# Optimization experiments

Hardware: AMD Instinct MI355X
Metric: run time of the kernel (lower is better)

Reference implementation:

```python
import jax, jax.numpy as jnp
import numpy as np
from jax import lax

DN = ('NHWC', 'HWIO', 'NHWC')

def _conv(a, w):
    return lax.conv_general_dilated(a, w, (1, 1), 'SAME', dimension_numbers=DN)

def _hard_sigmoid(z):
    return jnp.clip(0.2 * z + 0.5, 0.0, 1.0)


def setup_inputs() -> dict:
    key = jax.random.key(0)
    ks = jax.random.split(key, 4)
    B, T, H, W, C, F, K = 2, 16, 64, 64, 64, 64, 3
    x = jax.random.normal(ks[0], (B, T, H, W, C), dtype=jnp.float32)
    Wx = jax.random.normal(ks[1], (K, K, C, 4 * F), dtype=jnp.float32) * (2.0 / (K * K * C)) ** 0.5
    Wh = jax.random.normal(ks[2], (K, K, F, 4 * F), dtype=jnp.float32) * (2.0 / (K * K * F)) ** 0.5
    b = jax.random.normal(ks[3], (4 * F,), dtype=jnp.float32) * 0.01
    gamma = jnp.ones((F,), dtype=jnp.float32)
    beta = jnp.zeros((F,), dtype=jnp.float32)
    moving_mean = jnp.zeros((F,), dtype=jnp.float32)
    moving_var = jnp.ones((F,), dtype=jnp.float32)
    return {"x": x, "Wx": Wx, "Wh": Wh, "b": b, "gamma": gamma,
            "beta": beta, "moving_mean": moving_mean, "moving_var": moving_var}


def reference(x, Wx, Wh, b, gamma, beta, moving_mean, moving_var):
    B, T, H, W, C = x.shape
    F = Wh.shape[2]
    # Precompute the input-to-gate convolutions for all timesteps in one big conv.
    xg = _conv(x.reshape(B * T, H, W, C), Wx) + b          # (B*T, H, W, 4F)
    xg = xg.reshape(B, T, H, W, 4 * F).transpose(1, 0, 2, 3, 4)  # (T, B, H, W, 4F)

    h0 = jnp.zeros((B, H, W, F), dtype=x.dtype)
    c0 = jnp.zeros((B, H, W, F), dtype=x.dtype)

    def step(carry, xt):
        h, c = carry
        z = xt + _conv(h, Wh)                               # (B, H, W, 4F)
        zi, zf, zg, zo = jnp.split(z, 4, axis=-1)           # Keras gate order: i, f, c, o
        i = _hard_sigmoid(zi)
        f = _hard_sigmoid(zf)
        g = jnp.tanh(zg)
        o = _hard_sigmoid(zo)
        c_new = f * c + i * g
        h_new = o * jnp.tanh(c_new)
        return (h_new, c_new), h_new

    _, hs = lax.scan(step, (h0, c0), xg)                    # (T, B, H, W, F)
    out = hs.transpose(1, 0, 2, 3, 4)                       # (B, T, H, W, F)

    # BatchNormalization in inference mode (training=False), eps=1e-3 (Keras default)
    eps = 1e-3
    inv = gamma * lax.rsqrt(moving_var + eps)
    out = out * inv + (beta - moving_mean * inv)
    return out
```

## Files before the change

### kernel.cpp

```cpp
#include <hip/hip_runtime.h>
#include <cstddef>

typedef __attribute__((ext_vector_type(8))) _Float16 half8;
typedef __attribute__((ext_vector_type(4))) float f32x4;
typedef __attribute__((ext_vector_type(4))) unsigned short us4;

#define TT 16
#define APAD 72
#define A_TILE (3*34*APAD)
#define CHUNK  8192
#define NB     6
#define PF     5
#define XNB    4
#define XPF    3

__device__ __forceinline__ unsigned short f2h(float f) {
    return __builtin_bit_cast(unsigned short, (_Float16)f);
}
__device__ __forceinline__ float h2f(unsigned short u) {
    return (float)__builtin_bit_cast(_Float16, u);
}
__device__ __forceinline__ float hsig(float z) {
    return fminf(fmaxf(0.2f * z + 0.5f, 0.f), 1.f);
}

__global__ __launch_bounds__(256) void prep_kernel(
    const float* __restrict__ Wx, const float* __restrict__ Wh,
    const float* __restrict__ gamma, const float* __restrict__ beta,
    const float* __restrict__ mean, const float* __restrict__ var,
    unsigned short* __restrict__ Wc, float* __restrict__ bn)
{
    if (blockIdx.x == 1152) {
        if (threadIdx.x < 64) {
            const int c = threadIdx.x;
            const float inv = gamma[c] * rsqrtf(var[c] + 1e-3f);
            bn[c] = inv;
            bn[64 + c] = beta[c] - mean[c] * inv;
        }
        return;
    }
    const int i = blockIdx.x * 256 + threadIdx.x;
    const int j  = i & 7;
    const int n  = (i >> 3) & 255;
    const int kg = (i >> 11) & 3;
    const int s  = i >> 13;
    const int sub = s % 18;
    const float* W = (s >= 18) ? Wh : Wx;
    const int k5 = sub * 32 + kg * 8 + j;
    const int c = k5 & 63, q = k5 >> 6;
    const int kx = q % 3, ky = q / 3;
    Wc[i] = f2h(W[(size_t)((ky * 3 + kx) * 64 + c) * 256 + n]);
}

#define BLOAD(slot, ci) {                                                     \
    const unsigned short* _p = Wc + (size_t)(ci) * CHUNK + boff;              \
    bp[slot][0] = *(const half8*)_p;                                          \
    bp[slot][1] = *(const half8*)(_p + 128);                                  \
}

template<int C0, int CLAST, int AOFF>
__device__ __forceinline__ void conv_pass18(
    const unsigned short* __restrict__ Wc, const int boff,
    half8 (&bp)[NB][2],
    const unsigned short* abase,
    f32x4 acc[2][2])
{
    #pragma unroll
    for (int sub = 0; sub < 18; ++sub) {
        const int ci = C0 + sub;
        if (ci + PF <= CLAST) BLOAD((ci + PF) % NB, ci + PF)

        const int ky = sub / 6, kx = (sub / 2) % 3, cb = sub & 1;
        const half8 b0 = bp[ci % NB][0];
        const half8 b1 = bp[ci % NB][1];
        const unsigned short* at = abase + AOFF + (ky * 34 + kx) * APAD + cb * 32;
        const half8 a0 = *(const half8*)(at);
        const half8 a1 = *(const half8*)(at + 16 * APAD);
        acc[0][0] = __builtin_amdgcn_mfma_f32_16x16x32_f16(a0, b0, acc[0][0], 0, 0, 0);
        acc[0][1] = __builtin_amdgcn_mfma_f32_16x16x32_f16(a0, b1, acc[0][1], 0, 0, 0);
        acc[1][0] = __builtin_amdgcn_mfma_f32_16x16x32_f16(a1, b0, acc[1][0], 0, 0, 0);
        acc[1][1] = __builtin_amdgcn_mfma_f32_16x16x32_f16(a1, b1, acc[1][1], 0, 0, 0);
    }
}

__global__ __launch_bounds__(512) void xconv_kernel(
    const float* __restrict__ x,
    const unsigned short* __restrict__ Wc,
    const float* __restrict__ bias,
    unsigned short* __restrict__ xg)
{
    const int bid0 = blockIdx.x;
    const int bid = (bid0 & 7) * 256 + (bid0 >> 3);
    const int y = bid & 63;
    const int t = (bid >> 6) & 15;
    const int n = bid >> 10;
    const int tid = threadIdx.x, lane = tid & 63, w = tid >> 6;
    const int p0 = lane & 15, g = lane >> 4;

    __shared__ __align__(16) unsigned short smem[3 * 66 * APAD];

    const int boff = g * 2048 + (w * 32 + p0) * 8;

    half8 bp[XNB][2];
    #pragma unroll
    for (int sc = 0; sc < XPF; ++sc) BLOAD(sc, sc)

    const float* __restrict__ xt = x + (size_t)(n * TT + t) * 4096 * 64;
    for (int idx = tid; idx < 3 * 66 * 8; idx += 512) {
        const int cg  = idx & 7;
        const int col = (idx >> 3) % 66;
        const int r   = (idx >> 3) / 66;
        const int gy = y + r - 1;
        const int gx = col - 1;
        const bool ok = ((unsigned)gy < 64u) && ((unsigned)gx < 64u);
        float4 v0 = make_float4(0.f, 0.f, 0.f, 0.f), v1 = v0;
        if (ok) {
            const float* p = xt + (size_t)(gy * 64 + gx) * 64 + cg * 8;
            v0 = *(const float4*)p;
            v1 = *(const float4*)(p + 4);
        }
        __align__(16) unsigned short os[8];
        os[0] = f2h(v0.x); os[1] = f2h(v0.y); os[2] = f2h(v0.z); os[3] = f2h(v0.w);
        os[4] = f2h(v1.x); os[5] = f2h(v1.y); os[6] = f2h(v1.z); os[7] = f2h(v1.w);
        *(uint4*)&smem[(r * 66 + col) * APAD + cg * 8] = *(const uint4*)os;
    }
    __syncthreads();

    const unsigned short* abase = smem + p0 * APAD + g * 8;

    f32x4 acc[4][2] = {};
    #pragma unroll
    for (int sub = 0; sub < 18; ++sub) {
        if (sub + XPF < 18) BLOAD((sub + XPF) % XNB, sub + XPF)

        const int ky = sub / 6, kx = (sub / 2) % 3, cb = sub & 1;
        const half8 b0 = bp[sub % XNB][0];
        const half8 b1 = bp[sub % XNB][1];
        #pragma unroll
        for (int cq = 0; cq < 4; ++cq) {
            const half8 a = *(const half8*)(abase
                + (ky * 66 + cq * 16 + kx) * APAD + cb * 32);
            acc[cq][0] = __builtin_amdgcn_mfma_f32_16x16x32_f16(a, b0, acc[cq][0], 0, 0, 0);
            acc[cq][1] = __builtin_amdgcn_mfma_f32_16x16x32_f16(a, b1, acc[cq][1], 0, 0, 0);
        }
    }

    const float bv0 = bias[w * 32 + p0];
    const float bv1 = bias[w * 32 + 16 + p0];
    #pragma unroll
    for (int xh2 = 0; xh2 < 2; ++xh2) {
        unsigned short os[16];
        #pragma unroll
        for (int mfc = 0; mfc < 2; ++mfc)
            #pragma unroll
            for (int nf = 0; nf < 2; ++nf)
                #pragma unroll
                for (int j = 0; j < 4; ++j)
                    os[mfc * 8 + nf * 4 + j] =
                        f2h(acc[xh2 * 2 + mfc][nf][j] + (nf ? bv1 : bv0));
        const size_t vi = ((((size_t)(n * TT + t) * 64 + y) * 2 + xh2) * 8 + w) * 64 + lane;
        unsigned short* dst = xg + vi * 16;
        *(uint4*)dst       = *(uint4*)&os[0];
        *(uint4*)(dst + 8) = *(uint4*)&os[8];
    }
}

template<int FUSED>
__global__ __launch_bounds__(512) void convstep_kernel(
    const float* __restrict__ x,
    const unsigned short* __restrict__ hb,
    const unsigned short* __restrict__ Wc,
    const float* __restrict__ bias,
    const unsigned short* __restrict__ xg,
    float* __restrict__ cbuf,
    unsigned short* __restrict__ ho,
    const float* __restrict__ bn,
    float* __restrict__ out,
    const int t)
{
    const int bid0 = blockIdx.x;
    const int bid = (bid0 & 7) * 32 + (bid0 >> 3);
    const int xh = bid & 1;
    const int y  = (bid >> 1) & 63;
    const int n  = bid >> 7;
    const int tid = threadIdx.x;
    const int lane = tid & 63;
    const int w = tid >> 6;
    const int p0 = lane & 15;
    const int g  = lane >> 4;

    constexpr int SMEM_SHORTS = FUSED ? (2 * A_TILE) : 17408;
    __shared__ __align__(16) unsigned short smem[SMEM_SHORTS];

    const int boff = g * 2048 + (w * 32 + p0) * 8;
    const bool do_h = FUSED || (t > 0);

    unsigned short xs[16];
    if (!FUSED) {
        const size_t vi = ((((size_t)(n * TT + t) * 64 + y) * 2 + xh) * 8 + w) * 64 + lane;
        const uint4* xp = (const uint4*)(xg + vi * 16);
        *(uint4*)&xs[0] = xp[0];
        *(uint4*)&xs[8] = xp[1];
    }

    f32x4 acc[2][2] = {};
    if (do_h) {
        constexpr int C0 = FUSED ? 0 : 18;
        half8 bp[NB][2];
        #pragma unroll
        for (int sc = 0; sc < PF; ++sc) BLOAD((C0 + sc) % NB, C0 + sc)

        constexpr int NTILE = FUSED ? 2 : 1;
        const float* __restrict__ xt = x + (size_t)(n * TT + t) * 4096 * 64;
        const size_t hbase = (size_t)n * 4096 * 64;
        for (int idx = tid; idx < NTILE * 3 * 34 * 8; idx += 512) {
            const int cg  = idx & 7;
            const int col = (idx >> 3) % 34;
            const int i3  = (idx >> 3) / 34;
            const int r   = i3 % 3;
            const int src = i3 / 3;
            const int gy = y + r - 1;
            const int gx = xh * 32 + col - 1;
            const bool ok = ((unsigned)gy < 64u) && ((unsigned)gx < 64u);
            const int ebase = (r * 34 + col) * APAD + cg * 8;
            if (FUSED && src == 0) {
                float4 v0 = make_float4(0.f, 0.f, 0.f, 0.f), v1 = v0;
                if (ok) {
                    const float* p = xt + (size_t)(gy * 64 + gx) * 64 + cg * 8;
                    v0 = *(const float4*)p;
                    v1 = *(const float4*)(p + 4);
                }
                __align__(16) unsigned short os[8];
                os[0] = f2h(v0.x); os[1] = f2h(v0.y); os[2] = f2h(v0.z); os[3] = f2h(v0.w);
                os[4] = f2h(v1.x); os[5] = f2h(v1.y); os[6] = f2h(v1.z); os[7] = f2h(v1.w);
                *(uint4*)&smem[ebase] = *(const uint4*)os;
            } else {
                uint4 v = make_uint4(0u, 0u, 0u, 0u);
                if (ok) v = *(const uint4*)(hb + hbase + (size_t)(gy * 64 + gx) * 64 + cg * 8);
                *(uint4*)&smem[(FUSED ? A_TILE : 0) + ebase] = v;
            }
        }
        __syncthreads();

        const unsigned short* abase = smem + p0 * APAD + g * 8;
        if (FUSED) {
            conv_pass18<0, 35, 0>(Wc, boff, bp, abase, acc);
            conv_pass18<18, 35, A_TILE>(Wc, boff, bp, abase, acc);
        } else {
            conv_pass18<18, 35, 0>(Wc, boff, bp, abase, acc);
        }
    }

    __syncthreads();
    float* gbuf = (float*)smem;
    const int gate = w >> 1;
    const int chalf = (w & 1) * 32;

    float bv[2];
    bv[0] = bias[w * 32 + p0];
    bv[1] = bias[w * 32 + 16 + p0];

    #pragma unroll
    for (int mf = 0; mf < 2; ++mf)
        #pragma unroll
        for (int nf = 0; nf < 2; ++nf)
            #pragma unroll
            for (int j = 0; j < 4; ++j) {
                float v = acc[mf][nf][j] + (FUSED ? bv[nf] : h2f(xs[mf * 8 + nf * 4 + j]));
                v = (gate == 2) ? tanhf(v) : hsig(v);
                const int px = mf * 16 + g * 4 + j;
                gbuf[(gate * 32 + px) * 68 + chalf + nf * 16 + p0] = v;
            }
    __syncthreads();

    const int p  = tid >> 4;
    const int c4 = (tid & 15) * 4;
    const float4 iv = *(const float4*)&gbuf[(0 * 32 + p) * 68 + c4];
    const float4 fv = *(const float4*)&gbuf[(1 * 32 + p) * 68 + c4];
    const float4 gv = *(const float4*)&gbuf[(2 * 32 + p) * 68 + c4];
    const float4 ov = *(const float4*)&gbuf[(3 * 32 + p) * 68 + c4];
    const size_t gpix = (size_t)((n * 64 + y) * 64 + xh * 32 + p);
    const size_t sb = gpix * 64 + c4;
    const float4 cold = do_h ? *(const float4*)&cbuf[sb]
                             : make_float4(0.f, 0.f, 0.f, 0.f);
    const float4 scv  = *(const float4*)&bn[c4];
    const float4 shv  = *(const float4*)&bn[64 + c4];

    const float ivv[4] = {iv.x, iv.y, iv.z, iv.w};
    const float fvv[4] = {fv.x, fv.y, fv.z, fv.w};
    const float gvv[4] = {gv.x, gv.y, gv.z, gv.w};
    const float ovv[4] = {ov.x, ov.y, ov.z, ov.w};
    const float cov[4] = {cold.x, cold.y, cold.z, cold.w};
    const float scc[4] = {scv.x, scv.y, scv.z, scv.w};
    const float shh[4] = {shv.x, shv.y, shv.z, shv.w};

    float cnew[4], obuf[4];
    us4 hh;
    unsigned short* hhp = (unsigned short*)&hh;
    #pragma unroll
    for (int j = 0; j < 4; ++j) {
        const float cn = fvv[j] * cov[j] + ivv[j] * gvv[j];
        const float hn = ovv[j] * tanhf(cn);
        cnew[j] = cn;
        hhp[j] = f2h(hn);
        obuf[j] = hn * scc[j] + shh[j];
    }
    *(float4*)&cbuf[sb] = *(float4*)&cnew[0];
    *(us4*)&ho[sb]      = hh;
    const size_t ob = ((size_t)((n * TT + t) * 4096 + y * 64 + xh * 32 + p)) * 64 + c4;
    *(float4*)&out[ob] = *(float4*)&obuf[0];
}

extern "C" void kernel_launch(void* const* d_in, const int* in_sizes, int n_in,
                              void* d_out, int out_size, void* d_ws, size_t ws_size,
                              hipStream_t stream) {
    const float* x     = (const float*)d_in[0];
    const float* Wx    = (const float*)d_in[1];
    const float* Wh    = (const float*)d_in[2];
    const float* b     = (const float*)d_in[3];
    const float* gamma = (const float*)d_in[4];
    const float* beta  = (const float*)d_in[5];
    const float* mean  = (const float*)d_in[6];
    const float* var   = (const float*)d_in[7];
    float* out = (float*)d_out;
    char* ws = (char*)d_ws;

    unsigned short* Wc   = (unsigned short*)(ws);
    float*          bn   = (float*)(ws + 589824);
    unsigned short* hA   = (unsigned short*)(ws + 590336);
    float*          cbuf = (float*)(ws + 1638912);
    unsigned short* hB   = (unsigned short*)(ws + 3736064);
    unsigned short* xg   = (unsigned short*)(ws + 4784640);
    const size_t NEED = 4784640ull + 67108864ull;

    prep_kernel<<<1153, 256, 0, stream>>>(Wx, Wh, gamma, beta, mean, var, Wc, bn);

    if (ws_size >= NEED) {
        xconv_kernel<<<2048, 512, 0, stream>>>(x, Wc, b, xg);
        for (int t = 0; t < TT; ++t) {
            const bool even = (t & 1) == 0;
            convstep_kernel<0><<<256, 512, 0, stream>>>(
                x, even ? hA : hB, Wc, b, xg, cbuf, even ? hB : hA, bn, out, t);
        }
    } else {
        hipMemsetAsync(ws + 590336, 0, 3145728, stream);
        for (int t = 0; t < TT; ++t) {
            const bool even = (t & 1) == 0;
            convstep_kernel<1><<<256, 512, 0, stream>>>(
                x, even ? hA : hB, Wc, b, xg, cbuf, even ? hB : hA, bn, out, t);
        }
    }
}
```

Measured before the change: 199.0 us.

## Fuse first LSTM timestep into input-conv kernel and skip final state writes

Since h0 and c0 are zero, the t=0 gates depend only on the input convolution. The xconv kernel now computes the t=0 gate activations, cell state, hidden state and BN output directly, instead of writing xg for t=0. This removes one recurrent convstep launch and its h-convolution. The last timestep also skips writing c and h, which nothing reads afterwards. The cost is a larger shared buffer and extra epilogue work in the t=0 blocks of xconv, which may make those blocks uneven.

Result: no change. 196.7 us (-1.1%).

```diff
diff --git a/kernel.cpp b/kernel.cpp
--- a/kernel.cpp
+++ b/kernel.cpp
@@ -87,7 +87,11 @@
     const float* __restrict__ x,
     const unsigned short* __restrict__ Wc,
     const float* __restrict__ bias,
-    unsigned short* __restrict__ xg)
+    unsigned short* __restrict__ xg,
+    const float* __restrict__ bn,
+    float* __restrict__ cbuf,
+    unsigned short* __restrict__ h1,
+    float* __restrict__ out)
 {
     const int bid0 = blockIdx.x;
     const int bid = (bid0 & 7) * 256 + (bid0 >> 3);
@@ -97,7 +101,7 @@
     const int tid = threadIdx.x, lane = tid & 63, w = tid >> 6;
     const int p0 = lane & 15, g = lane >> 4;
 
-    __shared__ __align__(16) unsigned short smem[3 * 66 * APAD];
+    __shared__ __align__(16) unsigned short smem[17408];
 
     const int boff = g * 2048 + (w * 32 + p0) * 8;
 
@@ -147,21 +151,72 @@
 
     const float bv0 = bias[w * 32 + p0];
     const float bv1 = bias[w * 32 + 16 + p0];
-    #pragma unroll
-    for (int xh2 = 0; xh2 < 2; ++xh2) {
-        unsigned short os[16];
+
+    if (t != 0) {
         #pragma unroll
-        for (int mfc = 0; mfc < 2; ++mfc)
+        for (int xh2 = 0; xh2 < 2; ++xh2) {
+            unsigned short os[16];
             #pragma unroll
-            for (int nf = 0; nf < 2; ++nf)
+            for (int mfc = 0; mfc < 2; ++mfc)
                 #pragma unroll
-                for (int j = 0; j < 4; ++j)
-                    os[mfc * 8 + nf * 4 + j] =
-                        f2h(acc[xh2 * 2 + mfc][nf][j] + (nf ? bv1 : bv0));
-        const size_t vi = ((((size_t)(n * TT + t) * 64 + y) * 2 + xh2) * 8 + w) * 64 + lane;
-        unsigned short* dst = xg + vi * 16;
-        *(uint4*)dst       = *(uint4*)&os[0];
-        *(uint4*)(dst + 8) = *(uint4*)&os[8];
+                for (int nf = 0; nf < 2; ++nf)
+                    #pragma unroll
+                    for (int j = 0; j < 4; ++j)
+                        os[mfc * 8 + nf * 4 + j] =
+                            f2h(acc[xh2 * 2 + mfc][nf][j] + (nf ? bv1 : bv0));
+            const size_t vi = ((((size_t)(n * TT + t) * 64 + y) * 2 + xh2) * 8 + w) * 64 + lane;
+            unsigned short* dst = xg + vi * 16;
+            *(uint4*)dst       = *(uint4*)&os[0];
+            *(uint4*)(dst + 8) = *(uint4*)&os[8];
+        }
+    } else {
+        float* gbuf = (float*)smem;
+        const int gate = w >> 1;
+        const int chalf = (w & 1) * 32;
+        #pragma unroll
+        for (int xh2 = 0; xh2 < 2; ++xh2) {
+            __syncthreads();
+            #pragma unroll
+            for (int mf = 0; mf < 2; ++mf)
+                #pragma unroll
+                for (int nf = 0; nf < 2; ++nf)
+                    #pragma unroll
+                    for (int j = 0; j < 4; ++j) {
+                        float v = acc[xh2 * 2 + mf][nf][j] + (nf ? bv1 : bv0);
+                        v = (gate == 2) ? tanhf(v) : hsig(v);
+                        const int px = mf * 16 + g * 4 + j;
+                        gbuf[(gate * 32 + px) * 68 + chalf + nf * 16 + p0] = v;
+                    }
+            __syncthreads();
+            const int p  = tid >> 4;
+            const int c4 = (tid & 15) * 4;
+            const float4 iv = *(const float4*)&gbuf[(0 * 32 + p) * 68 + c4];
+            const float4 gv = *(const float4*)&gbuf[(2 * 32 + p) * 68 + c4];
+            const float4 ov = *(const float4*)&gbuf[(3 * 32 + p) * 68 + c4];
+            const float ivv[4] = {iv.x, iv.y, iv.z, iv.w};
+            const float gvv[4] = {gv.x, gv.y, gv.z, gv.w};
+            const float ovv[4] = {ov.x, ov.y, ov.z, ov.w};
+            const float4 scv = *(const float4*)&bn[c4];
+            const float4 shv = *(const float4*)&bn[64 + c4];
+            const float scc[4] = {scv.x, scv.y, scv.z, scv.w};
+            const float shh[4] = {shv.x, shv.y, shv.z, shv.w};
+            const size_t sb = ((size_t)((n * 64 + y) * 64 + xh2 * 32 + p)) * 64 + c4;
+            float cnew[4], obuf[4];
+            us4 hh;
+            unsigned short* hhp = (unsigned short*)&hh;
+            #pragma unroll
+            for (int j = 0; j < 4; ++j) {
+                const float cn = ivv[j] * gvv[j];
+                const float hn = ovv[j] * tanhf(cn);
+                cnew[j] = cn;
+                hhp[j] = f2h(hn);
+                obuf[j] = hn * scc[j] + shh[j];
+            }
+            *(float4*)&cbuf[sb] = *(float4*)&cnew[0];
+            *(us4*)&h1[sb]      = hh;
+            const size_t ob = ((size_t)((n * TT + 0) * 4096 + y * 64 + xh2 * 32 + p)) * 64 + c4;
+            *(float4*)&out[ob] = *(float4*)&obuf[0];
+        }
     }
 }
 
@@ -305,8 +360,10 @@
         hhp[j] = f2h(hn);
         obuf[j] = hn * scc[j] + shh[j];
     }
-    *(float4*)&cbuf[sb] = *(float4*)&cnew[0];
-    *(us4*)&ho[sb]      = hh;
+    if (t != TT - 1) {
+        *(float4*)&cbuf[sb] = *(float4*)&cnew[0];
+        *(us4*)&ho[sb]      = hh;
+    }
     const size_t ob = ((size_t)((n * TT + t) * 4096 + y * 64 + xh * 32 + p)) * 64 + c4;
     *(float4*)&out[ob] = *(float4*)&obuf[0];
 }
@@ -336,8 +393,8 @@
     prep_kernel<<<1153, 256, 0, stream>>>(Wx, Wh, gamma, beta, mean, var, Wc, bn);
 
     if (ws_size >= NEED) {
-        xconv_kernel<<<2048, 512, 0, stream>>>(x, Wc, b, xg);
-        for (int t = 0; t < TT; ++t) {
+        xconv_kernel<<<2048, 512, 0, stream>>>(x, Wc, b, xg, bn, cbuf, hB, out);
+        for (int t = 1; t < TT; ++t) {
             const bool even = (t & 1) == 0;
             convstep_kernel<0><<<256, 512, 0, stream>>>(
                 x, even ? hA : hB, Wc, b, xg, cbuf, even ? hB : hA, bn, out, t);
```

## Fold first timestep into input-conv kernel and skip dead final state writes

Applied to the files above, without the earlier changes.

Because h0 and c0 are zero, the t=0 gate pre-activations equal the input convolution plus bias. The input-conv kernel now computes the t=0 LSTM cell directly, staging gates through shared memory, and writes c, h and the normalized output itself. The recurrent loop then starts at t=1, removing one convstep launch and its hidden-state convolution. The last step also skips writing c and h, which are never read. The cost is extra shared-memory passes and syncs in the t=0 blocks of the input conv, which makes them slower than the other blocks.

After: 197.0 us, median of 2. Within noise of the previous version (-1.0%).

```diff
diff --git a/kernel.cpp b/kernel.cpp
--- a/kernel.cpp
+++ b/kernel.cpp
@@ -87,7 +87,11 @@
     const float* __restrict__ x,
     const unsigned short* __restrict__ Wc,
     const float* __restrict__ bias,
-    unsigned short* __restrict__ xg)
+    unsigned short* __restrict__ xg,
+    const float* __restrict__ bn,
+    float* __restrict__ cbuf,
+    unsigned short* __restrict__ h1,
+    float* __restrict__ out)
 {
     const int bid0 = blockIdx.x;
     const int bid = (bid0 & 7) * 256 + (bid0 >> 3);
@@ -147,21 +151,59 @@
 
     const float bv0 = bias[w * 32 + p0];
     const float bv1 = bias[w * 32 + 16 + p0];
-    #pragma unroll
-    for (int xh2 = 0; xh2 < 2; ++xh2) {
-        unsigned short os[16];
-        #pragma unroll
-        for (int mfc = 0; mfc < 2; ++mfc)
+
+    if (t != 0) {
+        #pragma unroll
+        for (int xh2 = 0; xh2 < 2; ++xh2) {
+            unsigned short os[16];
+            #pragma unroll
+            for (int mfc = 0; mfc < 2; ++mfc)
+                #pragma unroll
+                for (int nf = 0; nf < 2; ++nf)
+                    #pragma unroll
+                    for (int j = 0; j < 4; ++j)
+                        os[mfc * 8 + nf * 4 + j] =
+                            f2h(acc[xh2 * 2 + mfc][nf][j] + (nf ? bv1 : bv0));
+            const size_t vi = ((((size_t)(n * TT + t) * 64 + y) * 2 + xh2) * 8 + w) * 64 + lane;
+            unsigned short* dst = xg + vi * 16;
+            *(uint4*)dst       = *(uint4*)&os[0];
+            *(uint4*)(dst + 8) = *(uint4*)&os[8];
+        }
+    } else {
+        float* gbuf = (float*)smem;
+        const int gate = w >> 1;
+        const int chalf = (w & 1) * 32;
+        const int p  = tid >> 5;
+        const int c2 = (tid & 31) * 2;
+        #pragma unroll
+        for (int cq = 0; cq < 4; ++cq) {
+            __syncthreads();
             #pragma unroll
             for (int nf = 0; nf < 2; ++nf)
                 #pragma unroll
-                for (int j = 0; j < 4; ++j)
-                    os[mfc * 8 + nf * 4 + j] =
-                        f2h(acc[xh2 * 2 + mfc][nf][j] + (nf ? bv1 : bv0));
-        const size_t vi = ((((size_t)(n * TT + t) * 64 + y) * 2 + xh2) * 8 + w) * 64 + lane;
-        unsigned short* dst = xg + vi * 16;
-        *(uint4*)dst       = *(uint4*)&os[0];
-        *(uint4*)(dst + 8) = *(uint4*)&os[8];
+                for (int j = 0; j < 4; ++j) {
+                    float v = acc[cq][nf][j] + (nf ? bv1 : bv0);
+                    v = (gate == 2) ? tanhf(v) : hsig(v);
+                    const int px = g * 4 + j;
+                    gbuf[(gate * 16 + px) * 68 + chalf + nf * 16 + p0] = v;
+                }
+            __syncthreads();
+            const float2 iv = *(const float2*)&gbuf[(0 * 16 + p) * 68 + c2];
+            const float2 gv = *(const float2*)&gbuf[(2 * 16 + p) * 68 + c2];
+            const float2 ov = *(const float2*)&gbuf[(3 * 16 + p) * 68 + c2];
+            const float2 scv = *(const float2*)&bn[c2];
+            const float2 shv = *(const float2*)&bn[64 + c2];
+            const float cn0 = iv.x * gv.x;
+            const float cn1 = iv.y * gv.y;
+            const float hn0 = ov.x * tanhf(cn0);
+            const float hn1 = ov.y * tanhf(cn1);
+            const size_t sb = ((size_t)((n * 64 + y) * 64 + cq * 16 + p)) * 64 + c2;
+            *(float2*)&cbuf[sb] = make_float2(cn0, cn1);
+            const unsigned int hh = (unsigned int)f2h(hn0) | ((unsigned int)f2h(hn1) << 16);
+            *(unsigned int*)&h1[sb] = hh;
+            const size_t ob = ((size_t)((n * TT + 0) * 4096 + y * 64 + cq * 16 + p)) * 64 + c2;
+            *(float2*)&out[ob] = make_float2(hn0 * scv.x + shv.x, hn1 * scv.y + shv.y);
+        }
     }
 }
 
@@ -305,8 +347,10 @@
         hhp[j] = f2h(hn);
         obuf[j] = hn * scc[j] + shh[j];
     }
-    *(float4*)&cbuf[sb] = *(float4*)&cnew[0];
-    *(us4*)&ho[sb]      = hh;
+    if (t != TT - 1) {
+        *(float4*)&cbuf[sb] = *(float4*)&cnew[0];
+        *(us4*)&ho[sb]      = hh;
+    }
     const size_t ob = ((size_t)((n * TT + t) * 4096 + y * 64 + xh * 32 + p)) * 64 + c4;
     *(float4*)&out[ob] = *(float4*)&obuf[0];
 }
@@ -336,8 +380,8 @@
     prep_kernel<<<1153, 256, 0, stream>>>(Wx, Wh, gamma, beta, mean, var, Wc, bn);
 
     if (ws_size >= NEED) {
-        xconv_kernel<<<2048, 512, 0, stream>>>(x, Wc, b, xg);
-        for (int t = 0; t < TT; ++t) {
+        xconv_kernel<<<2048, 512, 0, stream>>>(x, Wc, b, xg, bn, cbuf, hB, out);
+        for (int t = 1; t < TT; ++t) {
             const bool even = (t & 1) == 0;
             convstep_kernel<0><<<256, 512, 0, stream>>>(
                 x, even ? hA : hB, Wc, b, xg, cbuf, even ? hB : hA, bn, out, t);
```
